# Performance work log

Hardware: AMD Instinct MI355X
Metric: run time of the kernel (lower is better)

The kernel has to match this reference:

```python
import jax, jax.numpy as jnp
import numpy as np

# irreps_in = irreps_out = "32x0e + 16x1o"; irreps_edge = "1x0e + 1x1o"
N_SCAL, N_VEC = 32, 16
RADIAL_EMBED, HIDDEN = 64, 64
# FullyConnectedTensorProduct instructions (uvw), v == 1 since edge mults are 1:
#  P1: 0e x 0e -> 0e (32*32)   P2: 1o x 1o -> 0e (16*32)
#  P3: 0e x 1o -> 1o (32*16)   P4: 1o x 0e -> 1o (16*16)   P5: 1o x 1o -> 1o (16*16)
SPLITS = np.cumsum([0, 32 * 32, 16 * 32, 32 * 16, 16 * 16, 16 * 16])
W_NUMEL = int(SPLITS[-1])  # 2560
SILU_NORM = 1.6790425  # e3nn normalize2mom constant for silu
# path weights: alpha = ir_out.dim / sum(num_elements over paths into same output)
PW0 = (1.0 / (32.0 + 16.0)) ** 0.5          # scalar output paths
PW1 = (3.0 / (32.0 + 16.0 + 16.0)) ** 0.5   # vector output paths
INV_SQRT3 = 3.0 ** -0.5  # wigner_3j(0,1,1)/(1,0,1)/(1,1,0) magnitude
INV_SQRT6 = 6.0 ** -0.5  # wigner_3j(1,1,1) = eps_ijk / sqrt(6)
N_NODES, N_EDGES = 8192, 65536


def radial_net(e, W0, W1, W2):
    # e3nn FullyConnectedNet: x @ (W / sqrt(fan_in)), normalized silu between layers
    h = e
    for W in (W0, W1):
        h = jax.nn.silu(h @ (W / jnp.sqrt(jnp.float32(W.shape[0])))) * SILU_NORM
    return h @ (W2 / jnp.sqrt(jnp.float32(W2.shape[0])))


def setup_inputs() -> dict:
    key = jax.random.key(0)
    ks = jax.random.split(key, 9)
    edge_index = jax.random.randint(ks[0], (2, N_EDGES), 0, N_NODES)
    node_feat = jax.random.normal(ks[1], (N_NODES, N_SCAL + 3 * N_VEC), jnp.float32)
    edge_feat = jax.random.normal(ks[2], (N_EDGES, 4), jnp.float32)
    edge_embed = jax.random.normal(ks[3], (N_EDGES, RADIAL_EMBED), jnp.float32)
    W_fc0 = jax.random.normal(ks[4], (RADIAL_EMBED, HIDDEN), jnp.float32)
    W_fc1 = jax.random.normal(ks[5], (HIDDEN, HIDDEN), jnp.float32)
    W_fc2 = jax.random.normal(ks[6], (HIDDEN, W_NUMEL), jnp.float32)
    Wsc0 = jax.random.normal(ks[7], (N_SCAL, N_SCAL), jnp.float32)
    Wsc1 = jax.random.normal(ks[8], (N_VEC, N_VEC), jnp.float32)
    return dict(edge_index=edge_index, node_feat=node_feat, edge_feat=edge_feat,
                edge_embed=edge_embed, dim_size=N_NODES,
                W_fc0=W_fc0, W_fc1=W_fc1, W_fc2=W_fc2, Wsc0=Wsc0, Wsc1=Wsc1)


def reference(edge_index, node_feat, edge_feat, edge_embed, dim_size,
              W_fc0, W_fc1, W_fc2, Wsc0, Wsc1):
    src, dst = edge_index[0], edge_index[1]
    w = radial_net(edge_embed, W_fc0, W_fc1, W_fc2)  # [E, 2560]
    W1 = w[:, SPLITS[0]:SPLITS[1]].reshape(-1, 32, 32)
    W2 = w[:, SPLITS[1]:SPLITS[2]].reshape(-1, 16, 32)
    W3 = w[:, SPLITS[2]:SPLITS[3]].reshape(-1, 32, 16)
    W4 = w[:, SPLITS[3]:SPLITS[4]].reshape(-1, 16, 16)
    W5 = w[:, SPLITS[4]:SPLITS[5]].reshape(-1, 16, 16)
    xe = node_feat[src]                                    # gather [E, 80]
    x0 = xe[:, :N_SCAL]                                    # [E, 32]
    x1 = xe[:, N_SCAL:].reshape(-1, N_VEC, 3)              # [E, 16, 3]
    y0, y1 = edge_feat[:, 0], edge_feat[:, 1:4]            # [E], [E, 3]
    # scalar outputs
    dot = jnp.einsum('eui,ei->eu', x1, y1)
    out0 = PW0 * (jnp.einsum('euw,eu,e->ew', W1, x0, y0)
                  + INV_SQRT3 * jnp.einsum('euw,eu->ew', W2, dot))
    # vector outputs ((x cross y)_k = eps_ijk x_i y_j)
    cross = jnp.cross(x1, y1[:, None, :])
    out1 = PW1 * (INV_SQRT3 * jnp.einsum('euw,eu,ek->ewk', W3, x0, y1)
                  + INV_SQRT3 * jnp.einsum('euw,euk,e->ewk', W4, x1, y0)
                  + INV_SQRT6 * jnp.einsum('euw,euk->ewk', W5, cross))
    msg = jnp.concatenate([out0, out1.reshape(-1, 3 * N_VEC)], axis=1)  # [E, 80]
    agg = jax.ops.segment_sum(msg, dst, num_segments=dim_size)          # [N, 80]
    # self-connection: e3nn o3.Linear applied per irrep, / sqrt(fan_in)
    n0 = node_feat[:, :N_SCAL]
    n1 = node_feat[:, N_SCAL:].reshape(-1, N_VEC, 3)
    sc0 = n0 @ Wsc0 / jnp.sqrt(jnp.float32(N_SCAL))
    sc1 = jnp.einsum('nui,uv->nvi', n1, Wsc1) / jnp.sqrt(jnp.float32(N_VEC))
    sc = jnp.concatenate([sc0, sc1.reshape(-1, 3 * N_VEC)], axis=1)
    return agg + sc
```

## Files before the change

### kernel.cpp

```cpp
#include <hip/hip_runtime.h>

typedef unsigned short u16;
typedef __bf16 bf16x8 __attribute__((ext_vector_type(8)));
typedef float  f32x4  __attribute__((ext_vector_type(4)));

#define NEDGES 65536
#define NNODES 8192
#define EPB 32

#define PW0f       0.14433756729740643f
#define PW1f       0.21650635094610965f
#define INV_SQRT3f 0.5773502691896258f
#define INV_SQRT6f 0.4082482904638631f
#define SILU_NORMf 1.6790425f

#define WT2_OFF 0
#define WT0_OFF 163840
#define WT1_OFF 167936
#define WS_ELEMS 172032

#define HSTR 72

__device__ __forceinline__ float silu_n(float z) {
    return SILU_NORMf * z / (1.0f + __expf(-z));
}
__device__ __forceinline__ u16 f2bf(float f) {
    return __builtin_bit_cast(u16, (__bf16)f);
}
__device__ __forceinline__ float bf2f(u16 u) {
    unsigned v = ((unsigned)u) << 16;
    return __builtin_bit_cast(float, v);
}
__device__ __forceinline__ bf16x8 ld_bf8(const u16* p) {
    return *reinterpret_cast<const bf16x8*>(p);
}
__device__ __forceinline__ bf16x8 cvt_bf8(const float* p) {
    float4 a = *reinterpret_cast<const float4*>(p);
    float4 b = *reinterpret_cast<const float4*>(p + 4);
    bf16x8 r;
    r[0]=(__bf16)a.x; r[1]=(__bf16)a.y; r[2]=(__bf16)a.z; r[3]=(__bf16)a.w;
    r[4]=(__bf16)b.x; r[5]=(__bf16)b.y; r[6]=(__bf16)b.z; r[7]=(__bf16)b.w;
    return r;
}
#define MFMA16(A,B,C) __builtin_amdgcn_mfma_f32_16x16x32_bf16(A,B,C,0,0,0)

__global__ void k_prep(const float* __restrict__ Wfc0,
                       const float* __restrict__ Wfc1,
                       const float* __restrict__ Wfc2,
                       const float* __restrict__ node_feat,
                       const float* __restrict__ Wsc0,
                       const float* __restrict__ Wsc1,
                       u16* __restrict__ ws,
                       float* __restrict__ out)
{
    const int bid = blockIdx.x;
    if (bid < 672) {
        int gid = bid * 256 + threadIdx.x;
        if (gid < 163840) {
            int k = gid / 2560;
            int j = gid - k * 2560;
            float s;
            if (j < 1024)      s = PW0f;
            else if (j < 1536) s = PW0f * INV_SQRT3f;
            else if (j < 2304) s = PW1f * INV_SQRT3f;
            else               s = PW1f * INV_SQRT6f;
            ws[WT2_OFF + j * 64 + k] = f2bf(Wfc2[gid] * (0.125f * s));
        } else if (gid < WT1_OFF) {
            int i = gid - WT0_OFF;
            int k = i >> 6, n = i & 63;
            ws[WT0_OFF + n * 64 + k] = f2bf(Wfc0[i] * 0.125f);
        } else if (gid < WS_ELEMS) {
            int i = gid - WT1_OFF;
            int k = i >> 6, n = i & 63;
            ws[WT1_OFF + n * 64 + k] = f2bf(Wfc1[i] * 0.125f);
        }
    } else {
        int gid = (bid - 672) * 256 + threadIdx.x;
        if (gid >= NNODES * 80) return;
        int n = gid / 80;
        int s = gid - n * 80;
        const float* nf = node_feat + (size_t)n * 80;
        float r;
        if (s < 32) {
            float a = 0.f;
            #pragma unroll
            for (int u = 0; u < 32; ++u) a += nf[u] * Wsc0[u * 32 + s];
            r = a * 0.17677669529663687f;
        } else {
            int v = (s - 32) / 3;
            int k = (s - 32) - v * 3;
            float a = 0.f;
            #pragma unroll
            for (int u = 0; u < 16; ++u) a += nf[32 + u * 3 + k] * Wsc1[u * 16 + v];
            r = a * 0.25f;
        }
        out[gid] = r;
    }
}

__global__ __launch_bounds__(256, 4) void k_main(
    const int*   __restrict__ eidx,
    const float* __restrict__ node_feat,
    const float* __restrict__ edge_feat,
    const float* __restrict__ edge_embed,
    const u16*   __restrict__ ws,
    float*       __restrict__ out)
{
    __shared__ __align__(16) char smem[20992];
    u16*   h1S  = (u16*)(smem);
    u16*   h0S  = (u16*)(smem + 4608);
    u16*   c12S = (u16*)(smem + 9216);
    u16*   x0S  = (u16*)(smem + 12288);
    u16*   cw45 = (u16*)(smem + 14336);
    float* y1S  = (float*)(smem + 20480);
    int*   dstS = (int*)(smem + 20864);
    float* msgS = (float*)(smem + 4608);

    const int t    = threadIdx.x;
    const int lane = t & 63;
    const int l15  = lane & 15;
    const int lq   = lane >> 4;
    const int wid  = t >> 6;
    const int role = (wid + blockIdx.x) & 3;
    const int eg0  = blockIdx.x * EPB;

    const u16* WT2 = ws + WT2_OFF;

    if (wid < 2) {
        const u16* WT0 = ws + WT0_OFF;
        const u16* WT1 = ws + WT1_OFF;
        const float* erow = edge_embed + (size_t)(eg0 + wid * 16 + l15) * 64 + 8 * lq;
        bf16x8 eB0 = cvt_bf8(erow);
        bf16x8 eB1 = cvt_bf8(erow + 32);
        #pragma unroll
        for (int ntl = 0; ntl < 4; ++ntl) {
            const u16* a = WT0 + (ntl * 16 + l15) * 64 + 8 * lq;
            bf16x8 A0 = ld_bf8(a);
            bf16x8 A1 = ld_bf8(a + 32);
            f32x4 z = {0.f, 0.f, 0.f, 0.f};
            z = MFMA16(A0, eB0, z);
            f32x4 dd = MFMA16(A1, eB1, z);
            ushort4 pk;
            pk.x = f2bf(silu_n(dd[0]));
            pk.y = f2bf(silu_n(dd[1]));
            pk.z = f2bf(silu_n(dd[2]));
            pk.w = f2bf(silu_n(dd[3]));
            *(ushort4*)&h0S[(wid * 16 + l15) * HSTR + ntl * 16 + lq * 4] = pk;
        }
        const u16* hrow = h0S + (wid * 16 + l15) * HSTR + 8 * lq;
        bf16x8 hB0 = ld_bf8(hrow);
        bf16x8 hB1 = ld_bf8(hrow + 32);
        #pragma unroll
        for (int ntl = 0; ntl < 4; ++ntl) {
            const u16* a = WT1 + (ntl * 16 + l15) * 64 + 8 * lq;
            bf16x8 A0 = ld_bf8(a);
            bf16x8 A1 = ld_bf8(a + 32);
            f32x4 z = {0.f, 0.f, 0.f, 0.f};
            z = MFMA16(A0, hB0, z);
            f32x4 dd = MFMA16(A1, hB1, z);
            ushort4 pk;
            pk.x = f2bf(silu_n(dd[0]));
            pk.y = f2bf(silu_n(dd[1]));
            pk.z = f2bf(silu_n(dd[2]));
            pk.w = f2bf(silu_n(dd[3]));
            *(ushort4*)&h1S[(wid * 16 + l15) * HSTR + ntl * 16 + lq * 4] = pk;
        }
    } else {
        const int t2  = t - 128;
        const int e   = t2 & 31;
        const int q   = t2 >> 5;
        const int eg  = eg0 + e;
        const int src = eidx[eg];
        const float* nf = node_feat + (size_t)src * 80;
        const float* ef = edge_feat + (size_t)eg * 4;
        if (q == 0) {
            dstS[e] = eidx[NEDGES + eg];
            const float y0 = ef[0];
            y1S[e] = ef[1]; y1S[32 + e] = ef[2]; y1S[64 + e] = ef[3];
            #pragma unroll
            for (int u = 0; u < 32; ++u) c12S[u * 32 + e] = f2bf(nf[u] * y0);
        } else if (q == 1) {
            const float ya = ef[1], yb = ef[2], yc = ef[3];
            #pragma unroll
            for (int u = 0; u < 16; ++u) {
                float d = nf[32 + u * 3] * ya + nf[32 + u * 3 + 1] * yb
                        + nf[32 + u * 3 + 2] * yc;
                c12S[(32 + u) * 32 + e] = f2bf(d);
            }
            #pragma unroll
            for (int u = 0; u < 32; ++u) x0S[u * 32 + e] = f2bf(nf[u]);
        } else if (q == 2) {
            const float y0 = ef[0];
            #pragma unroll
            for (int u = 0; u < 16; ++u) {
                cw45[(u * 3 + 0) * 32 + e] = f2bf(nf[32 + u * 3 + 0] * y0);
                cw45[(u * 3 + 1) * 32 + e] = f2bf(nf[32 + u * 3 + 1] * y0);
                cw45[(u * 3 + 2) * 32 + e] = f2bf(nf[32 + u * 3 + 2] * y0);
            }
        } else {
            const float ya = ef[1], yb = ef[2], yc = ef[3];
            #pragma unroll
            for (int u = 0; u < 16; ++u) {
                const float xa = nf[32 + u * 3], xb = nf[32 + u * 3 + 1], xc = nf[32 + u * 3 + 2];
                cw45[(48 + u * 3 + 0) * 32 + e] = f2bf(xb * yc - xc * yb);
                cw45[(48 + u * 3 + 1) * 32 + e] = f2bf(xc * ya - xa * yc);
                cw45[(48 + u * 3 + 2) * 32 + e] = f2bf(xa * yb - xb * ya);
            }
        }
    }
    __syncthreads();

    bf16x8 hb[2][2];
    #pragma unroll
    for (int eg = 0; eg < 2; ++eg) {
        const u16* r = h1S + (eg * 16 + l15) * HSTR + 8 * lq;
        hb[eg][0] = ld_bf8(r);
        hb[eg][1] = ld_bf8(r + 32);
    }

    float acc[32];
    #pragma unroll
    for (int i = 0; i < 32; ++i) acc[i] = 0.f;

    int t0, ntile;
    if      (role == 0) { t0 = 0;   ntile = 48; }
    else if (role == 1) { t0 = 48;  ntile = 48; }
    else if (role == 2) { t0 = 96;  ntile = 40; }
    else                { t0 = 136; ntile = 24; }

    const u16* Aw = WT2 + l15 * 64 + 8 * lq;

#define COMPUTE(A0_, A1_, D_)                                          \
    {                                                                  \
        _Pragma("unroll")                                              \
        for (int eg = 0; eg < 2; ++eg) {                               \
            f32x4 z = {0.f, 0.f, 0.f, 0.f};                            \
            z = MFMA16(A0_, hb[eg][0], z);                             \
            D_[eg] = MFMA16(A1_, hb[eg][1], z);                        \
        }                                                              \
    }

#define EPILOGUE(D_, TT_, HS_)                                               \
    {                                                                        \
        if ((TT_) < 96) {                         \
            const u16* cr = c12S + ((TT_) >> 1) * 32;                        \
            _Pragma("unroll")                                                \
            for (int eg = 0; eg < 2; ++eg) {                                 \
                const float c = bf2f(cr[eg * 16 + l15]);                     \
                _Pragma("unroll")                                            \
                for (int r = 0; r < 4; ++r)                                  \
                    acc[eg * 8 + (HS_) * 4 + r] += c * D_[eg][r];            \
            }                                                                \
        } else if ((TT_) < 128) {             \
            const u16* cr = x0S + ((TT_) - 96) * 32;                         \
            _Pragma("unroll")                                                \
            for (int eg = 0; eg < 2; ++eg) {                                 \
                const float c = bf2f(cr[eg * 16 + l15]);                     \
                _Pragma("unroll")                                            \
                for (int r = 0; r < 4; ++r)                                  \
                    acc[24 + eg * 4 + r] += c * D_[eg][r];                   \
            }                                                                \
        } else {                                   \
            const u16* cr = cw45 + ((TT_) - 128) * 96;                       \
            _Pragma("unroll")                                                \
            for (int eg = 0; eg < 2; ++eg) {                                 \
                const int e16 = eg * 16 + l15;                               \
                const float c0 = bf2f(cr[e16]);                              \
                const float c1 = bf2f(cr[32 + e16]);                         \
                const float c2 = bf2f(cr[64 + e16]);                         \
                _Pragma("unroll")                                            \
                for (int r = 0; r < 4; ++r) {                                \
                    const float dv = D_[eg][r];                              \
                    acc[eg * 12 + r * 3 + 0] += c0 * dv;                     \
                    acc[eg * 12 + r * 3 + 1] += c1 * dv;                     \
                    acc[eg * 12 + r * 3 + 2] += c2 * dv;                     \
                }                                                            \
            }                                                                \
        }                                                                    \
    }

    bf16x8 Aa0, Aa1, Ab0, Ab1;
    {
        const u16* p = Aw + (size_t)t0 * 1024;
        Aa0 = ld_bf8(p); Aa1 = ld_bf8(p + 32);
        const u16* q = Aw + (size_t)(t0 + 1) * 1024;
        Ab0 = ld_bf8(q); Ab1 = ld_bf8(q + 32);
    }
    const int np = ntile >> 1;
    #pragma unroll 1
    for (int p = 0; p < np; ++p) {
        const int tt = t0 + 2 * p;
        bf16x8 Ac0, Ac1, Ad0, Ad1;
        const bool more = (p + 1 < np);
        if (more) {
            const u16* q = Aw + (size_t)(tt + 2) * 1024;
            Ac0 = ld_bf8(q); Ac1 = ld_bf8(q + 32);
        }
        f32x4 d[2];
        COMPUTE(Aa0, Aa1, d);
        EPILOGUE(d, tt, 0);
        if (more) {
            const u16* q = Aw + (size_t)(tt + 3) * 1024;
            Ad0 = ld_bf8(q); Ad1 = ld_bf8(q + 32);
        }
        COMPUTE(Ab0, Ab1, d);
        EPILOGUE(d, tt + 1, 1);
        if (more) { Aa0 = Ac0; Aa1 = Ac1; Ab0 = Ad0; Ab1 = Ad1; }
    }
#undef COMPUTE
#undef EPILOGUE

    __syncthreads();
    if (role == 0) {
        #pragma unroll
        for (int eg = 0; eg < 2; ++eg) {
            float* mb = msgS + (eg * 16 + l15) * 81;
            #pragma unroll
            for (int hs = 0; hs < 2; ++hs)
                #pragma unroll
                for (int r = 0; r < 4; ++r)
                    mb[hs * 16 + lq * 4 + r] = acc[eg * 8 + hs * 4 + r];
        }
    } else if (role == 2) {
        #pragma unroll
        for (int eg = 0; eg < 2; ++eg) {
            const int e = eg * 16 + l15;
            const float w1x = y1S[e], w1y = y1S[32 + e], w1z = y1S[64 + e];
            float* mb = msgS + e * 81 + 32;
            #pragma unroll
            for (int r = 0; r < 4; ++r) {
                const float s = acc[24 + eg * 4 + r];
                mb[(lq * 4 + r) * 3 + 0] = acc[eg * 12 + r * 3 + 0] + s * w1x;
                mb[(lq * 4 + r) * 3 + 1] = acc[eg * 12 + r * 3 + 1] + s * w1y;
                mb[(lq * 4 + r) * 3 + 2] = acc[eg * 12 + r * 3 + 2] + s * w1z;
            }
        }
    }
    __syncthreads();
    if (role == 1) {
        #pragma unroll
        for (int eg = 0; eg < 2; ++eg) {
            float* mb = msgS + (eg * 16 + l15) * 81;
            #pragma unroll
            for (int hs = 0; hs < 2; ++hs)
                #pragma unroll
                for (int r = 0; r < 4; ++r)
                    mb[hs * 16 + lq * 4 + r] += acc[eg * 8 + hs * 4 + r];
        }
    } else if (role == 3) {
        #pragma unroll
        for (int eg = 0; eg < 2; ++eg) {
            float* mb = msgS + (eg * 16 + l15) * 81 + 32;
            #pragma unroll
            for (int r = 0; r < 4; ++r)
                #pragma unroll
                for (int k = 0; k < 3; ++k)
                    mb[(lq * 4 + r) * 3 + k] += acc[eg * 12 + r * 3 + k];
        }
    }
    __syncthreads();

    for (int idx = t; idx < EPB * 80; idx += 256) {
        const int e = idx / 80;
        const int s = idx - e * 80;
        atomicAdd(out + (size_t)dstS[e] * 80 + s, msgS[e * 81 + s]);
    }
}

extern "C" void kernel_launch(void* const* d_in, const int* in_sizes, int n_in,
                              void* d_out, int out_size, void* d_ws, size_t ws_size,
                              hipStream_t stream) {
    const int*   eidx       = (const int*)d_in[0];
    const float* node_feat  = (const float*)d_in[1];
    const float* edge_feat  = (const float*)d_in[2];
    const float* edge_embed = (const float*)d_in[3];
    const float* Wfc0       = (const float*)d_in[5];
    const float* Wfc1       = (const float*)d_in[6];
    const float* Wfc2       = (const float*)d_in[7];
    const float* Wsc0       = (const float*)d_in[8];
    const float* Wsc1       = (const float*)d_in[9];
    float* out = (float*)d_out;
    u16*   ws  = (u16*)d_ws;

    if (ws_size < (size_t)WS_ELEMS * sizeof(u16)) return;

    hipLaunchKernelGGL(k_prep, dim3(672 + 2560), dim3(256), 0, stream,
                       Wfc0, Wfc1, Wfc2, node_feat, Wsc0, Wsc1, ws, out);
    hipLaunchKernelGGL(k_main, dim3(NEDGES / EPB), dim3(256), 0, stream,
                       eidx, node_feat, edge_feat, edge_embed, ws, out);
}
```

Baseline: 110.0 us.

## Process 64 edges per block to reuse weight tiles across more edges

Doubles edges per block from 32 to 64, so each streamed bf16 weight tile of the radial output layer feeds four MFMA edge groups instead of two. All four waves now run the radial MLP first, then build the per-edge coefficients, and the work split across roles is rebalanced. The W4/W5 coefficients move to a padded ushort4 layout so they can be read as vector loads, and the message reduction gains an extra barrier stage. This cuts global weight traffic per edge and halves the number of blocks, at the cost of more LDS, more accumulator registers and possibly lower occupancy.

Result: slower. 133.9 us (+21.8%).

```diff
diff --git a/kernel.cpp b/kernel.cpp
--- a/kernel.cpp
+++ b/kernel.cpp
@@ -6,7 +6,7 @@
 
 #define NEDGES 65536
 #define NNODES 8192
-#define EPB 32
+#define EPB 64
 
 #define PW0f       0.14433756729740643f
 #define PW1f       0.21650635094610965f
@@ -106,15 +106,16 @@
     const u16*   __restrict__ ws,
     float*       __restrict__ out)
 {
-    __shared__ __align__(16) char smem[20992];
+    __shared__ __align__(16) char smem[36864];
     u16*   h1S  = (u16*)(smem);
-    u16*   h0S  = (u16*)(smem + 4608);
     u16*   c12S = (u16*)(smem + 9216);
-    u16*   x0S  = (u16*)(smem + 12288);
-    u16*   cw45 = (u16*)(smem + 14336);
-    float* y1S  = (float*)(smem + 20480);
-    int*   dstS = (int*)(smem + 20864);
-    float* msgS = (float*)(smem + 4608);
+    u16*   x0S  = (u16*)(smem + 15360);
+    u16*   w4S  = (u16*)(smem + 19456);
+    u16*   w5S  = (u16*)(smem + 27648);
+    float* y1S  = (float*)(smem + 35840);
+    int*   dstS = (int*)(smem + 36608);
+    u16*   h0S  = (u16*)(smem + 9216);
+    float* msgS = (float*)(smem);
 
     const int t    = threadIdx.x;
     const int lane = t & 63;
@@ -125,10 +126,10 @@
     const int eg0  = blockIdx.x * EPB;
 
     const u16* WT2 = ws + WT2_OFF;
-
-    if (wid < 2) {
-        const u16* WT0 = ws + WT0_OFF;
-        const u16* WT1 = ws + WT1_OFF;
+    const u16* WT0 = ws + WT0_OFF;
+    const u16* WT1 = ws + WT1_OFF;
+
+    {
         const float* erow = edge_embed + (size_t)(eg0 + wid * 16 + l15) * 64 + 8 * lq;
         bf16x8 eB0 = cvt_bf8(erow);
         bf16x8 eB1 = cvt_bf8(erow + 32);
@@ -147,6 +148,8 @@
             pk.w = f2bf(silu_n(dd[3]));
             *(ushort4*)&h0S[(wid * 16 + l15) * HSTR + ntl * 16 + lq * 4] = pk;
         }
+    }
+    {
         const u16* hrow = h0S + (wid * 16 + l15) * HSTR + 8 * lq;
         bf16x8 hB0 = ld_bf8(hrow);
         bf16x8 hB1 = ld_bf8(hrow + 32);
@@ -165,10 +168,12 @@
             pk.w = f2bf(silu_n(dd[3]));
             *(ushort4*)&h1S[(wid * 16 + l15) * HSTR + ntl * 16 + lq * 4] = pk;
         }
-    } else {
-        const int t2  = t - 128;
-        const int e   = t2 & 31;
-        const int q   = t2 >> 5;
+    }
+    __syncthreads();
+
+    {
+        const int e   = t & 63;
+        const int q   = t >> 6;
         const int eg  = eg0 + e;
         const int src = eidx[eg];
         const float* nf = node_feat + (size_t)src * 80;
@@ -176,64 +181,70 @@
         if (q == 0) {
             dstS[e] = eidx[NEDGES + eg];
             const float y0 = ef[0];
-            y1S[e] = ef[1]; y1S[32 + e] = ef[2]; y1S[64 + e] = ef[3];
-            #pragma unroll
-            for (int u = 0; u < 32; ++u) c12S[u * 32 + e] = f2bf(nf[u] * y0);
+            y1S[e] = ef[1]; y1S[64 + e] = ef[2]; y1S[128 + e] = ef[3];
+            #pragma unroll
+            for (int u = 0; u < 32; ++u) c12S[u * 64 + e] = f2bf(nf[u] * y0);
         } else if (q == 1) {
             const float ya = ef[1], yb = ef[2], yc = ef[3];
             #pragma unroll
             for (int u = 0; u < 16; ++u) {
                 float d = nf[32 + u * 3] * ya + nf[32 + u * 3 + 1] * yb
                         + nf[32 + u * 3 + 2] * yc;
-                c12S[(32 + u) * 32 + e] = f2bf(d);
+                c12S[(32 + u) * 64 + e] = f2bf(d);
             }
             #pragma unroll
-            for (int u = 0; u < 32; ++u) x0S[u * 32 + e] = f2bf(nf[u]);
+            for (int u = 0; u < 32; ++u) x0S[u * 64 + e] = f2bf(nf[u]);
         } else if (q == 2) {
             const float y0 = ef[0];
             #pragma unroll
             for (int u = 0; u < 16; ++u) {
-                cw45[(u * 3 + 0) * 32 + e] = f2bf(nf[32 + u * 3 + 0] * y0);
-                cw45[(u * 3 + 1) * 32 + e] = f2bf(nf[32 + u * 3 + 1] * y0);
-                cw45[(u * 3 + 2) * 32 + e] = f2bf(nf[32 + u * 3 + 2] * y0);
+                ushort4 pk;
+                pk.x = f2bf(nf[32 + u * 3 + 0] * y0);
+                pk.y = f2bf(nf[32 + u * 3 + 1] * y0);
+                pk.z = f2bf(nf[32 + u * 3 + 2] * y0);
+                pk.w = 0;
+                *(ushort4*)&w4S[(u * 64 + e) * 4] = pk;
             }
         } else {
             const float ya = ef[1], yb = ef[2], yc = ef[3];
             #pragma unroll
             for (int u = 0; u < 16; ++u) {
                 const float xa = nf[32 + u * 3], xb = nf[32 + u * 3 + 1], xc = nf[32 + u * 3 + 2];
-                cw45[(48 + u * 3 + 0) * 32 + e] = f2bf(xb * yc - xc * yb);
-                cw45[(48 + u * 3 + 1) * 32 + e] = f2bf(xc * ya - xa * yc);
-                cw45[(48 + u * 3 + 2) * 32 + e] = f2bf(xa * yb - xb * ya);
+                ushort4 pk;
+                pk.x = f2bf(xb * yc - xc * yb);
+                pk.y = f2bf(xc * ya - xa * yc);
+                pk.z = f2bf(xa * yb - xb * ya);
+                pk.w = 0;
+                *(ushort4*)&w5S[(u * 64 + e) * 4] = pk;
             }
         }
     }
     __syncthreads();
 
-    bf16x8 hb[2][2];
+    bf16x8 hb[4][2];
     #pragma unroll
-    for (int eg = 0; eg < 2; ++eg) {
+    for (int eg = 0; eg < 4; ++eg) {
         const u16* r = h1S + (eg * 16 + l15) * HSTR + 8 * lq;
         hb[eg][0] = ld_bf8(r);
         hb[eg][1] = ld_bf8(r + 32);
     }
 
-    float acc[32];
+    float acc[48];
     #pragma unroll
-    for (int i = 0; i < 32; ++i) acc[i] = 0.f;
+    for (int i = 0; i < 48; ++i) acc[i] = 0.f;
 
     int t0, ntile;
-    if      (role == 0) { t0 = 0;   ntile = 48; }
-    else if (role == 1) { t0 = 48;  ntile = 48; }
-    else if (role == 2) { t0 = 96;  ntile = 40; }
-    else                { t0 = 136; ntile = 24; }
+    if      (role == 0) { t0 = 0;   ntile = 44; }
+    else if (role == 1) { t0 = 44;  ntile = 44; }
+    else if (role == 2) { t0 = 88;  ntile = 40; }
+    else                { t0 = 128; ntile = 32; }
 
     const u16* Aw = WT2 + l15 * 64 + 8 * lq;
 
 #define COMPUTE(A0_, A1_, D_)                                          \
     {                                                                  \
         _Pragma("unroll")                                              \
-        for (int eg = 0; eg < 2; ++eg) {                               \
+        for (int eg = 0; eg < 4; ++eg) {                               \
             f32x4 z = {0.f, 0.f, 0.f, 0.f};                            \
             z = MFMA16(A0_, hb[eg][0], z);                             \
             D_[eg] = MFMA16(A1_, hb[eg][1], z);                        \
@@ -243,31 +254,32 @@
 #define EPILOGUE(D_, TT_, HS_)                                               \
     {                                                                        \
         if ((TT_) < 96) {                         \
-            const u16* cr = c12S + ((TT_) >> 1) * 32;                        \
+            const u16* cr = c12S + ((TT_) >> 1) * 64;                        \
             _Pragma("unroll")                                                \
-            for (int eg = 0; eg < 2; ++eg) {                                 \
+            for (int eg = 0; eg < 4; ++eg) {                                 \
                 const float c = bf2f(cr[eg * 16 + l15]);                     \
                 _Pragma("unroll")                                            \
                 for (int r = 0; r < 4; ++r)                                  \
                     acc[eg * 8 + (HS_) * 4 + r] += c * D_[eg][r];            \
             }                                                                \
         } else if ((TT_) < 128) {             \
-            const u16* cr = x0S + ((TT_) - 96) * 32;                         \
+            const u16* cr = x0S + ((TT_) - 96) * 64;                         \
             _Pragma("unroll")                                                \
-            for (int eg = 0; eg < 2; ++eg) {                                 \
+            for (int eg = 0; eg < 4; ++eg) {                                 \
                 const float c = bf2f(cr[eg * 16 + l15]);                     \
                 _Pragma("unroll")                                            \
                 for (int r = 0; r < 4; ++r)                                  \
-                    acc[24 + eg * 4 + r] += c * D_[eg][r];                   \
+                    acc[32 + eg * 4 + r] += c * D_[eg][r];                   \
             }                                                                \
         } else {                                   \
-            const u16* cr = cw45 + ((TT_) - 128) * 96;                       \
+            const u16* cr = ((TT_) < 144 ? w4S + ((TT_) - 128) * 256         \
+                                         : w5S + ((TT_) - 144) * 256);       \
             _Pragma("unroll")                                                \
-            for (int eg = 0; eg < 2; ++eg) {                                 \
-                const int e16 = eg * 16 + l15;                               \
-                const float c0 = bf2f(cr[e16]);                              \
-                const float c1 = bf2f(cr[32 + e16]);                         \
-                const float c2 = bf2f(cr[64 + e16]);                         \
+            for (int eg = 0; eg < 4; ++eg) {                                 \
+                const ushort4 cw = *(const ushort4*)&cr[(eg * 16 + l15) * 4];\
+                const float c0 = bf2f(cw.x);                                 \
+                const float c1 = bf2f(cw.y);                                 \
+                const float c2 = bf2f(cw.z);                                 \
                 _Pragma("unroll")                                            \
                 for (int r = 0; r < 4; ++r) {                                \
                     const float dv = D_[eg][r];                              \
@@ -296,7 +308,7 @@
             const u16* q = Aw + (size_t)(tt + 2) * 1024;
             Ac0 = ld_bf8(q); Ac1 = ld_bf8(q + 32);
         }
-        f32x4 d[2];
+        f32x4 d[4];
         COMPUTE(Aa0, Aa1, d);
         EPILOGUE(d, tt, 0);
         if (more) {
@@ -313,7 +325,7 @@
     __syncthreads();
     if (role == 0) {
         #pragma unroll
-        for (int eg = 0; eg < 2; ++eg) {
+        for (int eg = 0; eg < 4; ++eg) {
             float* mb = msgS + (eg * 16 + l15) * 81;
             #pragma unroll
             for (int hs = 0; hs < 2; ++hs)
@@ -321,25 +333,21 @@
                 for (int r = 0; r < 4; ++r)
                     mb[hs * 16 + lq * 4 + r] = acc[eg * 8 + hs * 4 + r];
         }
-    } else if (role == 2) {
-        #pragma unroll
-        for (int eg = 0; eg < 2; ++eg) {
-            const int e = eg * 16 + l15;
-            const float w1x = y1S[e], w1y = y1S[32 + e], w1z = y1S[64 + e];
-            float* mb = msgS + e * 81 + 32;
-            #pragma unroll
-            for (int r = 0; r < 4; ++r) {
-                const float s = acc[24 + eg * 4 + r];
-                mb[(lq * 4 + r) * 3 + 0] = acc[eg * 12 + r * 3 + 0] + s * w1x;
-                mb[(lq * 4 + r) * 3 + 1] = acc[eg * 12 + r * 3 + 1] + s * w1y;
-                mb[(lq * 4 + r) * 3 + 2] = acc[eg * 12 + r * 3 + 2] + s * w1z;
-            }
+    } else if (role == 3) {
+        #pragma unroll
+        for (int eg = 0; eg < 4; ++eg) {
+            float* mb = msgS + (eg * 16 + l15) * 81 + 32;
+            #pragma unroll
+            for (int r = 0; r < 4; ++r)
+                #pragma unroll
+                for (int k = 0; k < 3; ++k)
+                    mb[(lq * 4 + r) * 3 + k] = acc[eg * 12 + r * 3 + k];
         }
     }
     __syncthreads();
     if (role == 1) {
         #pragma unroll
-        for (int eg = 0; eg < 2; ++eg) {
+        for (int eg = 0; eg < 4; ++eg) {
             float* mb = msgS + (eg * 16 + l15) * 81;
             #pragma unroll
             for (int hs = 0; hs < 2; ++hs)
@@ -347,15 +355,31 @@
                 for (int r = 0; r < 4; ++r)
                     mb[hs * 16 + lq * 4 + r] += acc[eg * 8 + hs * 4 + r];
         }
-    } else if (role == 3) {
-        #pragma unroll
-        for (int eg = 0; eg < 2; ++eg) {
-            float* mb = msgS + (eg * 16 + l15) * 81 + 32;
-            #pragma unroll
-            for (int r = 0; r < 4; ++r)
+    } else if (role == 2) {
+        #pragma unroll
+        for (int eg = 0; eg < 4; ++eg) {
+            const int e = eg * 16 + l15;
+            const float w1x = y1S[e], w1y = y1S[64 + e], w1z = y1S[128 + e];
+            float* mb = msgS + e * 81 + 32;
+            #pragma unroll
+            for (int r = 0; r < 4; ++r) {
+                const float s = acc[32 + eg * 4 + r];
+                mb[(lq * 4 + r) * 3 + 0] += s * w1x;
+                mb[(lq * 4 + r) * 3 + 1] += s * w1y;
+                mb[(lq * 4 + r) * 3 + 2] += s * w1z;
+            }
+        }
+    }
+    __syncthreads();
+    if (role == 2) {
+        #pragma unroll
+        for (int eg = 0; eg < 4; ++eg) {
+            float* mb = msgS + (eg * 16 + l15) * 81;
+            #pragma unroll
+            for (int hs = 0; hs < 2; ++hs)
                 #pragma unroll
-                for (int k = 0; k < 3; ++k)
-                    mb[(lq * 4 + r) * 3 + k] += acc[eg * 12 + r * 3 + k];
+                for (int r = 0; r < 4; ++r)
+                    mb[hs * 16 + lq * 4 + r] += acc[eg * 8 + hs * 4 + r];
         }
     }
     __syncthreads();
```
